# Performance work log

Hardware: AMD Instinct MI355X
Metric: run time of the kernel (lower is better)

Reference implementation:

```python
import jax, jax.numpy as jnp
import numpy as np

D_MODEL = 2048
N_HEADS = 32
N_KV_HEADS = 8
HEAD_DIM = D_MODEL // N_HEADS
N_REP = N_HEADS // N_KV_HEADS
ROPE_BASE = 10000.0


def _rope_tables(seq_len, dim, dtype):
    inv_freq = 1.0 / (ROPE_BASE ** (jnp.arange(0, dim, 2, dtype=jnp.float32) / dim))
    t = jnp.arange(seq_len, dtype=jnp.float32)
    freqs = jnp.einsum('i,j->ij', t, inv_freq)          # [S, dim/2]
    emb = jnp.concatenate([freqs, freqs], axis=-1)      # [S, dim]
    return jnp.cos(emb).astype(dtype), jnp.sin(emb).astype(dtype)


def _apply_rotation(x, cos, sin):
    # x: [B, H, S, D]; cos/sin: [S, D] broadcast over B,H
    half = x.shape[-1] // 2
    x1, x2 = x[..., :half], x[..., half:]
    rot = jnp.concatenate([-x2, x1], axis=-1)
    return rot * sin + x * cos


def setup_inputs() -> dict:
    key = jax.random.key(0)
    kx, kq, kk, kv, ko = jax.random.split(key, 5)
    B, S = 2, 2048
    scale_in = 1.0 / np.sqrt(D_MODEL)
    x = jax.random.normal(kx, (B, S, D_MODEL), dtype=jnp.float32)
    Wq = jax.random.normal(kq, (N_HEADS * HEAD_DIM, D_MODEL), dtype=jnp.float32) * scale_in
    Wk = jax.random.normal(kk, (N_KV_HEADS * HEAD_DIM, D_MODEL), dtype=jnp.float32) * scale_in
    Wv = jax.random.normal(kv, (N_KV_HEADS * HEAD_DIM, D_MODEL), dtype=jnp.float32) * scale_in
    Wo = jax.random.normal(ko, (D_MODEL, N_HEADS * HEAD_DIM), dtype=jnp.float32) * scale_in
    # additive causal mask, broadcast over batch and heads
    neg = jnp.float32(-1e9)
    causal = jnp.triu(jnp.full((S, S), neg, dtype=jnp.float32), k=1)[None, None]
    return {"x": x, "Wq": Wq, "Wk": Wk, "Wv": Wv, "Wo": Wo, "mask": causal}


def reference(x, Wq, Wk, Wv, Wo, mask):
    B, S, _ = x.shape
    q = (x @ Wq.T).reshape(B, S, N_HEADS, HEAD_DIM).transpose(0, 2, 1, 3)      # [B,H,S,D]
    k = (x @ Wk.T).reshape(B, S, N_KV_HEADS, HEAD_DIM).transpose(0, 2, 1, 3)   # [B,Hkv,S,D]
    v = (x @ Wv.T).reshape(B, S, N_KV_HEADS, HEAD_DIM).transpose(0, 2, 1, 3)
    cos, sin = _rope_tables(S, HEAD_DIM, x.dtype)
    q = _apply_rotation(q, cos, sin)
    k = _apply_rotation(k, cos, sin)
    # repeat_kv: [B,Hkv,S,D] -> [B,Hkv*n_rep,S,D]
    k = jnp.repeat(k, N_REP, axis=1)
    v = jnp.repeat(v, N_REP, axis=1)
    scale = jnp.sqrt(jnp.float32(HEAD_DIM)).astype(x.dtype)
    scores = jnp.einsum('bhqd,bhkd->bhqk', q, k) / scale
    scores = scores + mask
    attn = jax.nn.softmax(scores.astype(jnp.float32), axis=-1).astype(q.dtype)
    out = jnp.einsum('bhqk,bhkd->bhqd', attn, v)
    out = out.transpose(0, 2, 1, 3).reshape(B, S, N_HEADS * HEAD_DIM)
    return out @ Wo.T
```

## Files before the change

kernel.cpp:

```cpp
#include <hip/hip_runtime.h>


typedef __bf16 bf16x8 __attribute__((ext_vector_type(8)));
typedef __bf16 bf16x4 __attribute__((ext_vector_type(4)));
typedef float f32x4 __attribute__((ext_vector_type(4)));

__device__ inline f32x4 mfma16(bf16x8 a, bf16x8 b, f32x4 c) {
    return __builtin_amdgcn_mfma_f32_16x16x32_bf16(a, b, c, 0, 0, 0);
}

__device__ inline void gld16(const __bf16* g, __bf16* l) {
    __builtin_amdgcn_global_load_lds(
        (const __attribute__((address_space(1))) void*)g,
        (__attribute__((address_space(3))) void*)l, 16, 0, 0);
}

__device__ inline bf16x4 pk4(float a, float b, float c, float d) {
    bf16x4 r; r[0] = (__bf16)a; r[1] = (__bf16)b; r[2] = (__bf16)c; r[3] = (__bf16)d;
    return r;
}

#define SCALE_Q 0.18033688011112042f
#define L2IF    0.4152410118609203f
#define INV2PI  0.15915494309189535f

__global__ void cvt4_kernel(const float* __restrict__ x,  const float* __restrict__ wq,
                            const float* __restrict__ wk, const float* __restrict__ wv,
                            __bf16* __restrict__ xb, __bf16* __restrict__ wqkvb)
{
    int i = blockIdx.x * blockDim.x + threadIdx.x;
    const float* src; __bf16* dst;
    if (i < 2097152)      { src = x  + (size_t)i * 4;  dst = xb + (size_t)i * 4; }
    else if (i < 3145728) { int j = i - 2097152; src = wq + (size_t)j * 4; dst = wqkvb + (size_t)j * 4; }
    else if (i < 3407872) { int j = i - 3145728; src = wk + (size_t)j * 4; dst = wqkvb + 4194304 + (size_t)j * 4; }
    else                  { int j = i - 3407872; src = wv + (size_t)j * 4; dst = wqkvb + 5242880 + (size_t)j * 4; }
    float4 f = *(const float4*)src;
    *(bf16x4*)dst = pk4(f.x, f.y, f.z, f.w);
}

__global__ void cvt_kernel(const float* __restrict__ in, __bf16* __restrict__ out, int n4)
{
    int i = blockIdx.x * blockDim.x + threadIdx.x;
    if (i >= n4) return;
    float4 f = ((const float4*)in)[i];
    ((bf16x4*)out)[i] = pk4(f.x, f.y, f.z, f.w);
}

template<bool ROPE, bool OUT_F32>
__global__ __launch_bounds__(512, 2) void gemm256(
    const __bf16* __restrict__ A, const __bf16* __restrict__ Bw,
    void* __restrict__ Cv, int M, int N, int K)
{
    __shared__ __bf16 LA[2][16384];
    __shared__ __bf16 LB[2][16384];
    const int tid  = threadIdx.x;
    const int lane = tid & 63;
    const int w    = tid >> 6;
    const int lm   = lane & 15;
    const int quad = lane >> 4;
    const int wr   = w >> 2;
    const int wc   = w & 3;

    int bx, by;
    {
        int nwg = gridDim.x * gridDim.y;
        int id  = blockIdx.x + gridDim.x * blockIdx.y;
        int q   = nwg >> 3;
        int swz = (id & 7) * q + (id >> 3);
        by = swz / gridDim.x;
        bx = swz - by * gridDim.x;
    }
    const int m0 = by * 256;
    const int n0 = bx * 256;
    const int NT = K >> 6;

    const int srow = tid >> 3;
    const int scol = ((tid & 7) ^ (srow & 7)) * 8;
    const int ldst = tid * 8;
    const __bf16* ga = A  + (size_t)(m0 + srow) * K + scol;
    const __bf16* gb = Bw + (size_t)(n0 + srow) * K + scol;

    auto STA = [&](int bf, int r, int u) {
        gld16(ga + (size_t)r * K + u * 64, &LA[bf][r * 64 + ldst]);
    };
    auto STB = [&](int bf, int r, int u) {
        gld16(gb + (size_t)r * K + u * 64, &LB[bf][r * 64 + ldst]);
    };

    f32x4 acc[8][4];
    #pragma unroll
    for (int i = 0; i < 8; ++i)
        #pragma unroll
        for (int j = 0; j < 4; ++j)
            acc[i][j] = (f32x4){0.f, 0.f, 0.f, 0.f};

    const int axo = (wr * 128 + lm) * 64;
    const int bxo = (wc * 64  + lm) * 64;
    const int ks0 = ((quad * 8)      ^ ((lm & 7) * 8));
    const int ks1 = ((32 + quad * 8) ^ ((lm & 7) * 8));

    STA(0, 0, 0); STA(0, 64, 0); STA(0, 128, 0); STA(0, 192, 0);
    STB(0, 0, 0); STB(0, 64, 0); STB(0, 128, 0); STB(0, 192, 0);
    STA(1, 0, 1); STA(1, 128, 1); STB(1, 0, 1); STA(1, 64, 1); STB(1, 64, 1);
    asm volatile("s_waitcnt vmcnt(5)" ::: "memory");
    __builtin_amdgcn_s_barrier();
    asm volatile("" ::: "memory");

    bf16x8 Af[4][2], Bf[4][2];
    for (int t = 0; t < NT; ++t) {
        const int b = t & 1;
        const __bf16* la = LA[b];
        const __bf16* lb = LB[b];
        #pragma unroll
        for (int mi = 0; mi < 4; ++mi) {
            Af[mi][0] = *(const bf16x8*)(la + axo + mi * 1024 + ks0);
            Af[mi][1] = *(const bf16x8*)(la + axo + mi * 1024 + ks1);
        }
        #pragma unroll
        for (int ni = 0; ni < 2; ++ni) {
            Bf[ni][0] = *(const bf16x8*)(lb + bxo + ni * 1024 + ks0);
            Bf[ni][1] = *(const bf16x8*)(lb + bxo + ni * 1024 + ks1);
        }
        if (t + 1 < NT) { STA(b ^ 1, 192, t + 1); STB(b ^ 1, 128, t + 1); }
        __builtin_amdgcn_s_barrier();
        asm volatile("s_waitcnt lgkmcnt(0)" ::: "memory");
        __builtin_amdgcn_s_setprio(1);
        #pragma unroll
        for (int mi = 0; mi < 4; ++mi)
            #pragma unroll
            for (int ni = 0; ni < 2; ++ni) {
                acc[mi][ni] = mfma16(Af[mi][0], Bf[ni][0], acc[mi][ni]);
                acc[mi][ni] = mfma16(Af[mi][1], Bf[ni][1], acc[mi][ni]);
            }
        __builtin_amdgcn_s_setprio(0);
        __builtin_amdgcn_s_barrier();
        #pragma unroll
        for (int ni = 2; ni < 4; ++ni) {
            Bf[ni][0] = *(const bf16x8*)(lb + bxo + ni * 1024 + ks0);
            Bf[ni][1] = *(const bf16x8*)(lb + bxo + ni * 1024 + ks1);
        }
        if (t + 1 < NT) STB(b ^ 1, 192, t + 1);
        if (t + 2 < NT) STA(b, 0, t + 2);
        __builtin_amdgcn_s_barrier();
        asm volatile("s_waitcnt lgkmcnt(0)" ::: "memory");
        __builtin_amdgcn_s_setprio(1);
        #pragma unroll
        for (int mi = 0; mi < 4; ++mi)
            #pragma unroll
            for (int ni = 2; ni < 4; ++ni) {
                acc[mi][ni] = mfma16(Af[mi][0], Bf[ni][0], acc[mi][ni]);
                acc[mi][ni] = mfma16(Af[mi][1], Bf[ni][1], acc[mi][ni]);
            }
        __builtin_amdgcn_s_setprio(0);
        __builtin_amdgcn_s_barrier();
        #pragma unroll
        for (int mi = 0; mi < 4; ++mi) {
            Af[mi][0] = *(const bf16x8*)(la + axo + (mi + 4) * 1024 + ks0);
            Af[mi][1] = *(const bf16x8*)(la + axo + (mi + 4) * 1024 + ks1);
        }
        if (t + 2 < NT) { STA(b, 128, t + 2); STB(b, 0, t + 2); }
        __builtin_amdgcn_s_barrier();
        asm volatile("s_waitcnt lgkmcnt(0)" ::: "memory");
        __builtin_amdgcn_s_setprio(1);
        #pragma unroll
        for (int mi = 0; mi < 4; ++mi)
            #pragma unroll
            for (int ni = 0; ni < 2; ++ni) {
                acc[mi + 4][ni] = mfma16(Af[mi][0], Bf[ni][0], acc[mi + 4][ni]);
                acc[mi + 4][ni] = mfma16(Af[mi][1], Bf[ni][1], acc[mi + 4][ni]);
            }
        __builtin_amdgcn_s_setprio(0);
        __builtin_amdgcn_s_barrier();
        if (t + 2 < NT) { STA(b, 64, t + 2); STB(b, 64, t + 2); }
        __builtin_amdgcn_s_barrier();
        __builtin_amdgcn_s_setprio(1);
        #pragma unroll
        for (int mi = 0; mi < 4; ++mi)
            #pragma unroll
            for (int ni = 2; ni < 4; ++ni) {
                acc[mi + 4][ni] = mfma16(Af[mi][0], Bf[ni][0], acc[mi + 4][ni]);
                acc[mi + 4][ni] = mfma16(Af[mi][1], Bf[ni][1], acc[mi + 4][ni]);
            }
        __builtin_amdgcn_s_setprio(0);
        if (t < NT - 2)       asm volatile("s_waitcnt vmcnt(5)" ::: "memory");
        else if (t == NT - 2) asm volatile("s_waitcnt vmcnt(0)" ::: "memory");
        __builtin_amdgcn_s_barrier();
        asm volatile("" ::: "memory");
    }

    float sc = 1.0f;
    if (ROPE) {
        const int colbase = n0 + wc * 64;
        const int region  = (colbase < 2048) ? 0 : (colbase < 2560 ? 1 : 2);
        if (region < 2) {
            if (region == 0) sc = SCALE_Q;
            float invr[2];
            invr[0] = exp2f(-(float)lm        * L2IF) * INV2PI;
            invr[1] = exp2f(-(float)(16 + lm) * L2IF) * INV2PI;
            #pragma unroll
            for (int i = 0; i < 8; ++i)
                #pragma unroll
                for (int r = 0; r < 4; ++r) {
                    float tt = (float)((m0 + wr * 128 + i * 16 + quad * 4 + r) & 2047);
                    #pragma unroll
                    for (int jp = 0; jp < 2; ++jp) {
                        float aR = tt * invr[jp];
                        aR -= floorf(aR);
                        float cs = __builtin_amdgcn_cosf(aR);
                        float sn = __builtin_amdgcn_sinf(aR);
                        float x1 = acc[i][jp][r], x2 = acc[i][jp + 2][r];
                        acc[i][jp][r]     = x1 * cs - x2 * sn;
                        acc[i][jp + 2][r] = x2 * cs + x1 * sn;
                    }
                }
        }
    }

    #pragma unroll
    for (int i = 0; i < 8; ++i)
        #pragma unroll
        for (int j = 0; j < 4; ++j)
            #pragma unroll
            for (int r = 0; r < 4; ++r) {
                int row = m0 + wr * 128 + i * 16 + quad * 4 + r;
                int col = n0 + wc * 64 + j * 16 + lm;
                if (OUT_F32)
                    ((float*)Cv)[(size_t)row * N + col] = acc[i][j][r];
                else
                    ((__bf16*)Cv)[(size_t)row * N + col] = (__bf16)(acc[i][j][r] * sc);
            }
}

#define BK 32

template<bool ROPE, bool OUT_F32>
__global__ __launch_bounds__(256) void gemm_bt(
    const __bf16* __restrict__ A, const __bf16* __restrict__ Bw,
    void* __restrict__ Cv, int M, int N, int K)
{
    __shared__ __bf16 As[128 * BK];
    __shared__ __bf16 Bs[128 * BK];
    const int tid  = threadIdx.x;
    const int lane = tid & 63;
    const int w    = tid >> 6;
    const int lm   = lane & 15;
    const int quad = lane >> 4;
    const int wm   = (w >> 1) * 64;
    const int wn   = (w & 1) * 64;

    int bx, by;
    {
        int id  = blockIdx.x + gridDim.x * blockIdx.y;
        int xcd = id & 7;
        int j   = id >> 3;
        by = xcd * 4 + (j & 3);
        bx = j >> 2;
    }
    const int m0 = by * 128;
    const int n0 = bx * 128;

    f32x4 acc[4][4];
    #pragma unroll
    for (int i = 0; i < 4; ++i)
        #pragma unroll
        for (int j = 0; j < 4; ++j)
            acc[i][j] = (f32x4){0.f, 0.f, 0.f, 0.f};

    const int srow = tid >> 2;
    const int sc8  = (tid & 3) * 8;
    const __bf16* gA0 = A  + (size_t)(m0 + srow) * K + sc8;
    const __bf16* gA1 = gA0 + (size_t)64 * K;
    const __bf16* gB0 = Bw + (size_t)(n0 + srow) * K + sc8;
    const __bf16* gB1 = gB0 + (size_t)64 * K;
    __bf16* lA0 = &As[srow * BK + sc8];
    __bf16* lA1 = &As[(srow + 64) * BK + sc8];
    __bf16* lB0 = &Bs[srow * BK + sc8];
    __bf16* lB1 = &Bs[(srow + 64) * BK + sc8];

    for (int k0 = 0; k0 < K; k0 += BK) {
        gld16(gA0 + k0, lA0);
        gld16(gA1 + k0, lA1);
        gld16(gB0 + k0, lB0);
        gld16(gB1 + k0, lB1);
        __syncthreads();

        bf16x8 af[4], bfr[4];
        #pragma unroll
        for (int i = 0; i < 4; ++i)
            af[i] = *(const bf16x8*)&As[(wm + i * 16 + lm) * BK + quad * 8];
        #pragma unroll
        for (int j = 0; j < 4; ++j)
            bfr[j] = *(const bf16x8*)&Bs[(wn + j * 16 + lm) * BK + quad * 8];
        #pragma unroll
        for (int i = 0; i < 4; ++i)
            #pragma unroll
            for (int j = 0; j < 4; ++j)
                acc[i][j] = mfma16(af[i], bfr[j], acc[i][j]);
        __syncthreads();
    }

    float sc = 1.0f;
    if (ROPE) {
        const int colbase = n0 + wn;
        const int region  = (colbase < 2048) ? 0 : (colbase < 2560 ? 1 : 2);
        if (region < 2) {
            if (region == 0) sc = SCALE_Q;
            float invr[2];
            invr[0] = exp2f(-(float)lm        * L2IF) * INV2PI;
            invr[1] = exp2f(-(float)(16 + lm) * L2IF) * INV2PI;
            #pragma unroll
            for (int i = 0; i < 4; ++i)
                #pragma unroll
                for (int r = 0; r < 4; ++r) {
                    float t = (float)((m0 + wm + i * 16 + quad * 4 + r) & 2047);
                    #pragma unroll
                    for (int jp = 0; jp < 2; ++jp) {
                        float a = t * invr[jp];
                        a -= floorf(a);
                        float cs = __builtin_amdgcn_cosf(a);
                        float sn = __builtin_amdgcn_sinf(a);
                        float x1 = acc[i][jp][r], x2 = acc[i][jp + 2][r];
                        acc[i][jp][r]     = x1 * cs - x2 * sn;
                        acc[i][jp + 2][r] = x2 * cs + x1 * sn;
                    }
                }
        }
    }

    #pragma unroll
    for (int i = 0; i < 4; ++i)
        #pragma unroll
        for (int j = 0; j < 4; ++j)
            #pragma unroll
            for (int r = 0; r < 4; ++r) {
                int row = m0 + wm + i * 16 + quad * 4 + r;
                int col = n0 + wn + j * 16 + lm;
                if (OUT_F32)
                    ((float*)Cv)[(size_t)row * N + col] = acc[i][j][r];
                else
                    ((__bf16*)Cv)[(size_t)row * N + col] = (__bf16)(acc[i][j][r] * sc);
            }
}

__global__ __launch_bounds__(256) void transpose_kernel(
    const __bf16* __restrict__ in, __bf16* __restrict__ out, int rowstride)
{
    __shared__ __bf16 T[64][72];
    const int t0 = blockIdx.x * 64;
    const int d0 = blockIdx.y * 64;
    const int r = threadIdx.x >> 2, c = (threadIdx.x & 3) * 16;
    *(int4*)&T[r][c]     = *(const int4*)(in + (size_t)(t0 + r) * rowstride + d0 + c);
    *(int4*)&T[r][c + 8] = *(const int4*)(in + (size_t)(t0 + r) * rowstride + d0 + c + 8);
    __syncthreads();
    bf16x8 o0, o1;
    #pragma unroll
    for (int i = 0; i < 8; ++i) { o0[i] = T[c + i][r]; o1[i] = T[c + 8 + i][r]; }
    *(bf16x8*)(out + (size_t)(d0 + r) * 4096 + t0 + c)     = o0;
    *(bf16x8*)(out + (size_t)(d0 + r) * 4096 + t0 + c + 8) = o1;
}

#define RS  72
#define PKS 72

__device__ inline void attn_tile(
    const bf16x8 (&qf)[2], f32x4 (&oacc)[4], float& l,
    int qbase, int k0, int w, int lm, int quad,
    const __bf16* Ks, const __bf16* Vs, __bf16* Ptw)
{
    f32x4 st[4];
    #pragma unroll
    for (int n = 0; n < 4; ++n)
        st[n] = (f32x4){0.f, 0.f, 0.f, 0.f};

    #pragma unroll
    for (int n = 0; n < 4; ++n) {
        bf16x8 kf0 = *(const bf16x8*)&Ks[(n * 16 + lm) * RS + quad * 8];
        bf16x8 kf1 = *(const bf16x8*)&Ks[(n * 16 + lm) * RS + 32 + quad * 8];
        st[n] = mfma16(kf0, qf[0], st[n]);
        st[n] = mfma16(kf1, qf[1], st[n]);
    }

    const int qi = qbase + w * 16 + lm;
    const bool any_mask = (k0 + 63 > qbase + w * 16);
    #pragma unroll
    for (int n = 0; n < 4; ++n) {
        const int kv0 = k0 + n * 16 + quad * 4;
        float e0, e1, e2, e3;
        if (any_mask) {
            e0 = (kv0     > qi) ? 0.f : __builtin_amdgcn_exp2f(st[n][0]);
            e1 = (kv0 + 1 > qi) ? 0.f : __builtin_amdgcn_exp2f(st[n][1]);
            e2 = (kv0 + 2 > qi) ? 0.f : __builtin_amdgcn_exp2f(st[n][2]);
            e3 = (kv0 + 3 > qi) ? 0.f : __builtin_amdgcn_exp2f(st[n][3]);
        } else {
            e0 = __builtin_amdgcn_exp2f(st[n][0]); e1 = __builtin_amdgcn_exp2f(st[n][1]);
            e2 = __builtin_amdgcn_exp2f(st[n][2]); e3 = __builtin_amdgcn_exp2f(st[n][3]);
        }
        l += (e0 + e1) + (e2 + e3);
        *(bf16x4*)&Ptw[lm * PKS + n * 16 + quad * 4] = pk4(e0, e1, e2, e3);
    }

    bf16x8 pf0 = *(const bf16x8*)&Ptw[lm * PKS + quad * 8];
    bf16x8 pf1 = *(const bf16x8*)&Ptw[lm * PKS + 32 + quad * 8];
    #pragma unroll
    for (int dt = 0; dt < 4; ++dt) {
        bf16x8 vf0 = *(const bf16x8*)&Vs[(dt * 16 + lm) * RS + quad * 8];
        bf16x8 vf1 = *(const bf16x8*)&Vs[(dt * 16 + lm) * RS + 32 + quad * 8];
        oacc[dt] = mfma16(vf0, pf0, oacc[dt]);
        oacc[dt] = mfma16(vf1, pf1, oacc[dt]);
    }
}

__device__ inline void attn_tile2(
    const bf16x8 (&qfA)[2], const bf16x8 (&qfB)[2],
    f32x4 (&oA)[4], f32x4 (&oB)[4], float& lA, float& lB,
    int qbA, int k0, int w, int lm, int quad,
    const __bf16* Ks, const __bf16* Vs, __bf16* PtA, __bf16* PtB)
{
    f32x4 stA[4], stB[4];
    #pragma unroll
    for (int n = 0; n < 4; ++n) {
        stA[n] = (f32x4){0.f, 0.f, 0.f, 0.f};
        stB[n] = (f32x4){0.f, 0.f, 0.f, 0.f};
    }

    #pragma unroll
    for (int n = 0; n < 4; ++n) {
        bf16x8 kf0 = *(const bf16x8*)&Ks[(n * 16 + lm) * RS + quad * 8];
        bf16x8 kf1 = *(const bf16x8*)&Ks[(n * 16 + lm) * RS + 32 + quad * 8];
        stB[n] = mfma16(kf0, qfB[0], stB[n]);
        stB[n] = mfma16(kf1, qfB[1], stB[n]);
        stA[n] = mfma16(kf0, qfA[0], stA[n]);
        stA[n] = mfma16(kf1, qfA[1], stA[n]);
    }

    #pragma unroll
    for (int n = 0; n < 4; ++n) {
        float e0 = __builtin_amdgcn_exp2f(stB[n][0]);
        float e1 = __builtin_amdgcn_exp2f(stB[n][1]);
        float e2 = __builtin_amdgcn_exp2f(stB[n][2]);
        float e3 = __builtin_amdgcn_exp2f(stB[n][3]);
        lB += (e0 + e1) + (e2 + e3);
        *(bf16x4*)&PtB[lm * PKS + n * 16 + quad * 4] = pk4(e0, e1, e2, e3);
    }

    const int qiA = qbA + w * 16 + lm;
    const bool maskA = (k0 + 63 > qbA + w * 16);
    #pragma unroll
    for (int n = 0; n < 4; ++n) {
        const int kv0 = k0 + n * 16 + quad * 4;
        float e0, e1, e2, e3;
        if (maskA) {
            e0 = (kv0     > qiA) ? 0.f : __builtin_amdgcn_exp2f(stA[n][0]);
            e1 = (kv0 + 1 > qiA) ? 0.f : __builtin_amdgcn_exp2f(stA[n][1]);
            e2 = (kv0 + 2 > qiA) ? 0.f : __builtin_amdgcn_exp2f(stA[n][2]);
            e3 = (kv0 + 3 > qiA) ? 0.f : __builtin_amdgcn_exp2f(stA[n][3]);
        } else {
            e0 = __builtin_amdgcn_exp2f(stA[n][0]); e1 = __builtin_amdgcn_exp2f(stA[n][1]);
            e2 = __builtin_amdgcn_exp2f(stA[n][2]); e3 = __builtin_amdgcn_exp2f(stA[n][3]);
        }
        lA += (e0 + e1) + (e2 + e3);
        *(bf16x4*)&PtA[lm * PKS + n * 16 + quad * 4] = pk4(e0, e1, e2, e3);
    }

    bf16x8 pB0 = *(const bf16x8*)&PtB[lm * PKS + quad * 8];
    bf16x8 pB1 = *(const bf16x8*)&PtB[lm * PKS + 32 + quad * 8];
    bf16x8 pA0 = *(const bf16x8*)&PtA[lm * PKS + quad * 8];
    bf16x8 pA1 = *(const bf16x8*)&PtA[lm * PKS + 32 + quad * 8];
    #pragma unroll
    for (int dt = 0; dt < 4; ++dt) {
        bf16x8 vf0 = *(const bf16x8*)&Vs[(dt * 16 + lm) * RS + quad * 8];
        bf16x8 vf1 = *(const bf16x8*)&Vs[(dt * 16 + lm) * RS + 32 + quad * 8];
        oB[dt] = mfma16(vf0, pB0, oB[dt]);
        oB[dt] = mfma16(vf1, pB1, oB[dt]);
        oA[dt] = mfma16(vf0, pA0, oA[dt]);
        oA[dt] = mfma16(vf1, pA1, oA[dt]);
    }
}

__device__ inline void attn_epilogue(
    f32x4 (&oacc)[4], float l,
    int qbase, int w, int lm, int quad, int b, int h, __bf16* o)
{
    float ls = l;
    ls += __shfl_xor(ls, 16);
    ls += __shfl_xor(ls, 32);
    float rinv = 1.0f / ls;
    const size_t rowbase = (size_t)(b * 2048 + qbase + w * 16 + lm) * 2048 + h * 64;
    #pragma unroll
    for (int dt = 0; dt < 4; ++dt) {
        *(bf16x4*)(o + rowbase + dt * 16 + quad * 4) =
            pk4(oacc[dt][0] * rinv, oacc[dt][1] * rinv,
                oacc[dt][2] * rinv, oacc[dt][3] * rinv);
    }
}

__global__ __launch_bounds__(512, 4) void attn_kernel(
    const __bf16* __restrict__ qkv, const __bf16* __restrict__ vt,
    __bf16* __restrict__ o)
{
    __shared__ __bf16 Ks[2][64 * RS];
    __shared__ __bf16 Vs[2][64 * RS];
    __shared__ __bf16 Pt[8][2][16 * PKS];
    const int tid  = threadIdx.x;
    const int w    = tid >> 6;
    const int lane = tid & 63;
    const int lm   = lane & 15;
    const int quad = lane >> 4;
    const int p = blockIdx.x, h = blockIdx.y, b = blockIdx.z;
    const int kvh = h >> 2;
    const int qbA = p * 128, qbB = (15 - p) * 128;
    const int ntA = 2 * p + 2, ntB = 32 - 2 * p;
    __bf16* PtwB = &Pt[w][0][0];
    __bf16* PtwA = &Pt[w][1][0];

    bf16x8 qfA[2], qfB[2];
    #pragma unroll
    for (int kh = 0; kh < 2; ++kh) {
        qfA[kh] = *(const bf16x8*)(qkv + (size_t)(b * 2048 + qbA + w * 16 + lm) * 3072
                                      + h * 64 + kh * 32 + quad * 8);
        qfB[kh] = *(const bf16x8*)(qkv + (size_t)(b * 2048 + qbB + w * 16 + lm) * 3072
                                      + h * 64 + kh * 32 + quad * 8);
    }

    f32x4 oA[4], oB[4];
    float lA = 0.f, lB = 0.f;
    #pragma unroll
    for (int j = 0; j < 4; ++j) {
        oA[j] = (f32x4){0.f, 0.f, 0.f, 0.f};
        oB[j] = (f32x4){0.f, 0.f, 0.f, 0.f};
    }

    const int srow = tid >> 3;
    const int scol = (tid & 7) * 8;
    const __bf16* kbase = qkv + (size_t)(b * 2048) * 3072 + 2048 + kvh * 64;
    const __bf16* vbase = vt  + (size_t)(kvh * 64 + srow) * 4096 + b * 2048;

    int4 kr0, vr0;
    kr0 = *(const int4*)(kbase + (size_t)srow * 3072 + scol);
    vr0 = *(const int4*)(vbase + scol);

    for (int kt = 0; kt < ntB; ++kt) {
        const int c = kt & 1;
        const int k0 = kt * 64;
        *(int4*)&Ks[c][srow * RS + scol] = kr0;
        *(int4*)&Vs[c][srow * RS + scol] = vr0;
        if (kt + 1 < ntB) {
            kr0 = *(const int4*)(kbase + (size_t)(k0 + 64 + srow) * 3072 + scol);
            vr0 = *(const int4*)(vbase + k0 + 64 + scol);
        }
        __syncthreads();
        if (kt < ntA)
            attn_tile2(qfA, qfB, oA, oB, lA, lB, qbA, k0, w, lm, quad,
                       Ks[c], Vs[c], PtwA, PtwB);
        else
            attn_tile(qfB, oB, lB, qbB, k0, w, lm, quad, Ks[c], Vs[c], PtwB);
    }

    attn_epilogue(oA, lA, qbA, w, lm, quad, b, h, o);
    attn_epilogue(oB, lB, qbB, w, lm, quad, b, h, o);
}

extern "C" void kernel_launch(void* const* d_in, const int* in_sizes, int n_in,
                              void* d_out, int out_size, void* d_ws, size_t ws_size,
                              hipStream_t stream)
{
    const float* x  = (const float*)d_in[0];
    const float* Wq = (const float*)d_in[1];
    const float* Wk = (const float*)d_in[2];
    const float* Wv = (const float*)d_in[3];
    const float* Wo = (const float*)d_in[4];

    const size_t Mi = 1u << 20;
    char* ob = (char*)d_out;
    __bf16* xb    = (__bf16*)ob;
    __bf16* wqkvb = (__bf16*)(ob + 16 * Mi);
    __bf16* vt    = (__bf16*)(ob + 28 * Mi);
    char* ws = (char*)d_ws;
    __bf16* qkvc = (__bf16*)ws;
    __bf16* aws  = (__bf16*)(ws + 24 * Mi);
    __bf16* wob  = (__bf16*)ws;

    dim3 blk(256);
    cvt4_kernel<<<14336, blk, 0, stream>>>(x, Wq, Wk, Wv, xb, wqkvb);
    gemm256<true, false><<<dim3(12, 16), dim3(512), 0, stream>>>(xb, wqkvb, qkvc, 4096, 3072, 2048);
    transpose_kernel<<<dim3(64, 8), blk, 0, stream>>>(qkvc + 2560, vt, 3072);
    attn_kernel<<<dim3(8, 32, 2), dim3(512), 0, stream>>>(qkvc, vt, aws);
    cvt_kernel<<<4096, blk, 0, stream>>>(Wo, wob, 1048576);
    gemm_bt<false, true><<<dim3(16, 32), blk, 0, stream>>>(aws, wob, d_out, 4096, 2048, 2048);
}
```

Baseline: 310.7 us.

## Rewrite output GEMM as double-buffered 256x128 kernel and XOR-swizzle attention LDS

```diff
diff --git a/kernel.cpp b/kernel.cpp
--- a/kernel.cpp
+++ b/kernel.cpp
@@ -231,33 +231,43 @@
             }
 }
 
-#define BK 32
-
-template<bool ROPE, bool OUT_F32>
-__global__ __launch_bounds__(256) void gemm_bt(
+__global__ __launch_bounds__(512, 2) void gemm_o(
     const __bf16* __restrict__ A, const __bf16* __restrict__ Bw,
-    void* __restrict__ Cv, int M, int N, int K)
-{
-    __shared__ __bf16 As[128 * BK];
-    __shared__ __bf16 Bs[128 * BK];
+    float* __restrict__ C, int M, int N, int K)
+{
+    __shared__ __bf16 LA[2][16384];
+    __shared__ __bf16 LB[2][8192];
     const int tid  = threadIdx.x;
     const int lane = tid & 63;
     const int w    = tid >> 6;
     const int lm   = lane & 15;
     const int quad = lane >> 4;
-    const int wm   = (w >> 1) * 64;
-    const int wn   = (w & 1) * 64;
+    const int wr   = w >> 1;
+    const int wc   = w & 1;
 
     int bx, by;
     {
         int id  = blockIdx.x + gridDim.x * blockIdx.y;
-        int xcd = id & 7;
-        int j   = id >> 3;
-        by = xcd * 4 + (j & 3);
-        bx = j >> 2;
-    }
-    const int m0 = by * 128;
+        int swz = (id & 7) * 32 + (id >> 3);
+        by = swz >> 4;
+        bx = swz & 15;
+    }
+    const int m0 = by * 256;
     const int n0 = bx * 128;
+    const int NT = K >> 6;
+
+    const int srow = tid >> 3;
+    const int scol = ((tid & 7) ^ (srow & 7)) * 8;
+    const int ldst = tid * 8;
+    const __bf16* ga = A  + (size_t)(m0 + srow) * K + scol;
+    const __bf16* gb = Bw + (size_t)(n0 + srow) * K + scol;
+
+    auto STA = [&](int bf, int r, int u) {
+        gld16(ga + (size_t)r * K + u * 64, &LA[bf][r * 64 + ldst]);
+    };
+    auto STB = [&](int bf, int r, int u) {
+        gld16(gb + (size_t)r * K + u * 64, &LB[bf][r * 64 + ldst]);
+    };
 
     f32x4 acc[4][4];
     #pragma unroll
@@ -266,79 +276,109 @@
         for (int j = 0; j < 4; ++j)
             acc[i][j] = (f32x4){0.f, 0.f, 0.f, 0.f};
 
-    const int srow = tid >> 2;
-    const int sc8  = (tid & 3) * 8;
-    const __bf16* gA0 = A  + (size_t)(m0 + srow) * K + sc8;
-    const __bf16* gA1 = gA0 + (size_t)64 * K;
-    const __bf16* gB0 = Bw + (size_t)(n0 + srow) * K + sc8;
-    const __bf16* gB1 = gB0 + (size_t)64 * K;
-    __bf16* lA0 = &As[srow * BK + sc8];
-    __bf16* lA1 = &As[(srow + 64) * BK + sc8];
-    __bf16* lB0 = &Bs[srow * BK + sc8];
-    __bf16* lB1 = &Bs[(srow + 64) * BK + sc8];
-
-    for (int k0 = 0; k0 < K; k0 += BK) {
-        gld16(gA0 + k0, lA0);
-        gld16(gA1 + k0, lA1);
-        gld16(gB0 + k0, lB0);
-        gld16(gB1 + k0, lB1);
-        __syncthreads();
-
-        bf16x8 af[4], bfr[4];
-        #pragma unroll
-        for (int i = 0; i < 4; ++i)
-            af[i] = *(const bf16x8*)&As[(wm + i * 16 + lm) * BK + quad * 8];
+    const int axo = (wr * 64 + lm) * 64;
+    const int bxo = (wc * 64 + lm) * 64;
+    const int ks0 = ((quad * 8)      ^ ((lm & 7) * 8));
+    const int ks1 = ((32 + quad * 8) ^ ((lm & 7) * 8));
+
+    STA(0, 0, 0); STA(0, 64, 0); STA(0, 128, 0); STA(0, 192, 0);
+    STB(0, 0, 0); STB(0, 64, 0);
+    STA(1, 0, 1); STA(1, 64, 1); STA(1, 128, 1); STA(1, 192, 1);
+    STB(1, 0, 1); STB(1, 64, 1);
+    asm volatile("s_waitcnt vmcnt(6)" ::: "memory");
+    __builtin_amdgcn_s_barrier();
+    asm volatile("" ::: "memory");
+
+    bf16x8 Af[4][2], Bf[4][2];
+    for (int t = 0; t < NT; ++t) {
+        const int b = t & 1;
+        const __bf16* la = LA[b];
+        const __bf16* lb = LB[b];
+        #pragma unroll
+        for (int mi = 0; mi < 2; ++mi) {
+            Af[mi][0] = *(const bf16x8*)(la + axo + mi * 1024 + ks0);
+            Af[mi][1] = *(const bf16x8*)(la + axo + mi * 1024 + ks1);
+        }
+        #pragma unroll
+        for (int ni = 0; ni < 2; ++ni) {
+            Bf[ni][0] = *(const bf16x8*)(lb + bxo + ni * 1024 + ks0);
+            Bf[ni][1] = *(const bf16x8*)(lb + bxo + ni * 1024 + ks1);
+        }
+        __builtin_amdgcn_s_barrier();
+        asm volatile("s_waitcnt lgkmcnt(0)" ::: "memory");
+        __builtin_amdgcn_s_setprio(1);
+        #pragma unroll
+        for (int mi = 0; mi < 2; ++mi)
+            #pragma unroll
+            for (int ni = 0; ni < 2; ++ni) {
+                acc[mi][ni] = mfma16(Af[mi][0], Bf[ni][0], acc[mi][ni]);
+                acc[mi][ni] = mfma16(Af[mi][1], Bf[ni][1], acc[mi][ni]);
+            }
+        __builtin_amdgcn_s_setprio(0);
+        __builtin_amdgcn_s_barrier();
+        #pragma unroll
+        for (int ni = 2; ni < 4; ++ni) {
+            Bf[ni][0] = *(const bf16x8*)(lb + bxo + ni * 1024 + ks0);
+            Bf[ni][1] = *(const bf16x8*)(lb + bxo + ni * 1024 + ks1);
+        }
+        __builtin_amdgcn_s_barrier();
+        asm volatile("s_waitcnt lgkmcnt(0)" ::: "memory");
+        __builtin_amdgcn_s_setprio(1);
+        #pragma unroll
+        for (int mi = 0; mi < 2; ++mi)
+            #pragma unroll
+            for (int ni = 2; ni < 4; ++ni) {
+                acc[mi][ni] = mfma16(Af[mi][0], Bf[ni][0], acc[mi][ni]);
+                acc[mi][ni] = mfma16(Af[mi][1], Bf[ni][1], acc[mi][ni]);
+            }
+        __builtin_amdgcn_s_setprio(0);
+        __builtin_amdgcn_s_barrier();
+        #pragma unroll
+        for (int mi = 2; mi < 4; ++mi) {
+            Af[mi][0] = *(const bf16x8*)(la + axo + mi * 1024 + ks0);
+            Af[mi][1] = *(const bf16x8*)(la + axo + mi * 1024 + ks1);
+        }
+        if (t + 2 < NT) { STB(b, 0, t + 2); STB(b, 64, t + 2); }
+        __builtin_amdgcn_s_barrier();
+        asm volatile("s_waitcnt lgkmcnt(0)" ::: "memory");
+        __builtin_amdgcn_s_setprio(1);
+        #pragma unroll
+        for (int mi = 2; mi < 4; ++mi)
+            #pragma unroll
+            for (int ni = 0; ni < 2; ++ni) {
+                acc[mi][ni] = mfma16(Af[mi][0], Bf[ni][0], acc[mi][ni]);
+                acc[mi][ni] = mfma16(Af[mi][1], Bf[ni][1], acc[mi][ni]);
+            }
+        __builtin_amdgcn_s_setprio(0);
+        __builtin_amdgcn_s_barrier();
+        if (t + 2 < NT) {
+            STA(b, 0, t + 2); STA(b, 64, t + 2);
+            STA(b, 128, t + 2); STA(b, 192, t + 2);
+        }
+        __builtin_amdgcn_s_setprio(1);
+        #pragma unroll
+        for (int mi = 2; mi < 4; ++mi)
+            #pragma unroll
+            for (int ni = 2; ni < 4; ++ni) {
+                acc[mi][ni] = mfma16(Af[mi][0], Bf[ni][0], acc[mi][ni]);
+                acc[mi][ni] = mfma16(Af[mi][1], Bf[ni][1], acc[mi][ni]);
+            }
+        __builtin_amdgcn_s_setprio(0);
+        if (t < NT - 2) asm volatile("s_waitcnt vmcnt(6)" ::: "memory");
+        else            asm volatile("s_waitcnt vmcnt(0)" ::: "memory");
+        __builtin_amdgcn_s_barrier();
+        asm volatile("" ::: "memory");
+    }
+
+    #pragma unroll
+    for (int i = 0; i < 4; ++i)
         #pragma unroll
         for (int j = 0; j < 4; ++j)
-            bfr[j] = *(const bf16x8*)&Bs[(wn + j * 16 + lm) * BK + quad * 8];
-        #pragma unroll
-        for (int i = 0; i < 4; ++i)
-            #pragma unroll
-            for (int j = 0; j < 4; ++j)
-                acc[i][j] = mfma16(af[i], bfr[j], acc[i][j]);
-        __syncthreads();
-    }
-
-    float sc = 1.0f;
-    if (ROPE) {
-        const int colbase = n0 + wn;
-        const int region  = (colbase < 2048) ? 0 : (colbase < 2560 ? 1 : 2);
-        if (region < 2) {
-            if (region == 0) sc = SCALE_Q;
-            float invr[2];
-            invr[0] = exp2f(-(float)lm        * L2IF) * INV2PI;
-            invr[1] = exp2f(-(float)(16 + lm) * L2IF) * INV2PI;
-            #pragma unroll
-            for (int i = 0; i < 4; ++i)
-                #pragma unroll
-                for (int r = 0; r < 4; ++r) {
-                    float t = (float)((m0 + wm + i * 16 + quad * 4 + r) & 2047);
-                    #pragma unroll
-                    for (int jp = 0; jp < 2; ++jp) {
-                        float a = t * invr[jp];
-                        a -= floorf(a);
-                        float cs = __builtin_amdgcn_cosf(a);
-                        float sn = __builtin_amdgcn_sinf(a);
-                        float x1 = acc[i][jp][r], x2 = acc[i][jp + 2][r];
-                        acc[i][jp][r]     = x1 * cs - x2 * sn;
-                        acc[i][jp + 2][r] = x2 * cs + x1 * sn;
-                    }
-                }
-        }
-    }
-
-    #pragma unroll
-    for (int i = 0; i < 4; ++i)
-        #pragma unroll
-        for (int j = 0; j < 4; ++j)
             #pragma unroll
             for (int r = 0; r < 4; ++r) {
-                int row = m0 + wm + i * 16 + quad * 4 + r;
-                int col = n0 + wn + j * 16 + lm;
-                if (OUT_F32)
-                    ((float*)Cv)[(size_t)row * N + col] = acc[i][j][r];
-                else
-                    ((__bf16*)Cv)[(size_t)row * N + col] = (__bf16)(acc[i][j][r] * sc);
+                int row = m0 + wr * 64 + i * 16 + quad * 4 + r;
+                int col = n0 + wc * 64 + j * 16 + lm;
+                C[(size_t)row * N + col] = acc[i][j][r];
             }
 }
 
@@ -359,14 +399,16 @@
     *(bf16x8*)(out + (size_t)(d0 + r) * 4096 + t0 + c + 8) = o1;
 }
 
-#define RS  72
-#define PKS 72
+#define RS  64
+#define PKS 64
 
 __device__ inline void attn_tile(
     const bf16x8 (&qf)[2], f32x4 (&oacc)[4], float& l,
     int qbase, int k0, int w, int lm, int quad,
     const __bf16* Ks, const __bf16* Vs, __bf16* Ptw)
 {
+    const int kb0 = (quad ^ (lm & 7)) * 8;
+    const int kb1 = ((quad + 4) ^ (lm & 7)) * 8;
     f32x4 st[4];
     #pragma unroll
     for (int n = 0; n < 4; ++n)
@@ -374,8 +416,8 @@
 
     #pragma unroll
     for (int n = 0; n < 4; ++n) {
-        bf16x8 kf0 = *(const bf16x8*)&Ks[(n * 16 + lm) * RS + quad * 8];
-        bf16x8 kf1 = *(const bf16x8*)&Ks[(n * 16 + lm) * RS + 32 + quad * 8];
+        bf16x8 kf0 = *(const bf16x8*)&Ks[(n * 16 + lm) * RS + kb0];
+        bf16x8 kf1 = *(const bf16x8*)&Ks[(n * 16 + lm) * RS + kb1];
         st[n] = mfma16(kf0, qf[0], st[n]);
         st[n] = mfma16(kf1, qf[1], st[n]);
     }
@@ -396,15 +438,16 @@
             e2 = __builtin_amdgcn_exp2f(st[n][2]); e3 = __builtin_amdgcn_exp2f(st[n][3]);
         }
         l += (e0 + e1) + (e2 + e3);
-        *(bf16x4*)&Ptw[lm * PKS + n * 16 + quad * 4] = pk4(e0, e1, e2, e3);
-    }
-
-    bf16x8 pf0 = *(const bf16x8*)&Ptw[lm * PKS + quad * 8];
-    bf16x8 pf1 = *(const bf16x8*)&Ptw[lm * PKS + 32 + quad * 8];
+        *(bf16x4*)&Ptw[lm * PKS + ((n * 4 + quad) ^ ((lm & 7) << 1)) * 4] =
+            pk4(e0, e1, e2, e3);
+    }
+
+    bf16x8 pf0 = *(const bf16x8*)&Ptw[lm * PKS + kb0];
+    bf16x8 pf1 = *(const bf16x8*)&Ptw[lm * PKS + kb1];
     #pragma unroll
     for (int dt = 0; dt < 4; ++dt) {
-        bf16x8 vf0 = *(const bf16x8*)&Vs[(dt * 16 + lm) * RS + quad * 8];
-        bf16x8 vf1 = *(const bf16x8*)&Vs[(dt * 16 + lm) * RS + 32 + quad * 8];
+        bf16x8 vf0 = *(const bf16x8*)&Vs[(dt * 16 + lm) * RS + kb0];
+        bf16x8 vf1 = *(const bf16x8*)&Vs[(dt * 16 + lm) * RS + kb1];
         oacc[dt] = mfma16(vf0, pf0, oacc[dt]);
         oacc[dt] = mfma16(vf1, pf1, oacc[dt]);
     }
@@ -416,6 +459,8 @@
     int qbA, int k0, int w, int lm, int quad,
     const __bf16* Ks, const __bf16* Vs, __bf16* PtA, __bf16* PtB)
 {
+    const int kb0 = (quad ^ (lm & 7)) * 8;
+    const int kb1 = ((quad + 4) ^ (lm & 7)) * 8;
     f32x4 stA[4], stB[4];
     #pragma unroll
     for (int n = 0; n < 4; ++n) {
@@ -425,8 +470,8 @@
 
     #pragma unroll
     for (int n = 0; n < 4; ++n) {
-        bf16x8 kf0 = *(const bf16x8*)&Ks[(n * 16 + lm) * RS + quad * 8];
-        bf16x8 kf1 = *(const bf16x8*)&Ks[(n * 16 + lm) * RS + 32 + quad * 8];
+        bf16x8 kf0 = *(const bf16x8*)&Ks[(n * 16 + lm) * RS + kb0];
+        bf16x8 kf1 = *(const bf16x8*)&Ks[(n * 16 + lm) * RS + kb1];
         stB[n] = mfma16(kf0, qfB[0], stB[n]);
         stB[n] = mfma16(kf1, qfB[1], stB[n]);
         stA[n] = mfma16(kf0, qfA[0], stA[n]);
@@ -440,7 +485,8 @@
         float e2 = __builtin_amdgcn_exp2f(stB[n][2]);
         float e3 = __builtin_amdgcn_exp2f(stB[n][3]);
         lB += (e0 + e1) + (e2 + e3);
-        *(bf16x4*)&PtB[lm * PKS + n * 16 + quad * 4] = pk4(e0, e1, e2, e3);
+        *(bf16x4*)&PtB[lm * PKS + ((n * 4 + quad) ^ ((lm & 7) << 1)) * 4] =
+            pk4(e0, e1, e2, e3);
     }
 
     const int qiA = qbA + w * 16 + lm;
@@ -459,17 +505,18 @@
             e2 = __builtin_amdgcn_exp2f(stA[n][2]); e3 = __builtin_amdgcn_exp2f(stA[n][3]);
         }
         lA += (e0 + e1) + (e2 + e3);
-        *(bf16x4*)&PtA[lm * PKS + n * 16 + quad * 4] = pk4(e0, e1, e2, e3);
-    }
-
-    bf16x8 pB0 = *(const bf16x8*)&PtB[lm * PKS + quad * 8];
-    bf16x8 pB1 = *(const bf16x8*)&PtB[lm * PKS + 32 + quad * 8];
-    bf16x8 pA0 = *(const bf16x8*)&PtA[lm * PKS + quad * 8];
-    bf16x8 pA1 = *(const bf16x8*)&PtA[lm * PKS + 32 + quad * 8];
+        *(bf16x4*)&PtA[lm * PKS + ((n * 4 + quad) ^ ((lm & 7) << 1)) * 4] =
+            pk4(e0, e1, e2, e3);
+    }
+
+    bf16x8 pB0 = *(const bf16x8*)&PtB[lm * PKS + kb0];
+    bf16x8 pB1 = *(const bf16x8*)&PtB[lm * PKS + kb1];
+    bf16x8 pA0 = *(const bf16x8*)&PtA[lm * PKS + kb0];
+    bf16x8 pA1 = *(const bf16x8*)&PtA[lm * PKS + kb1];
     #pragma unroll
     for (int dt = 0; dt < 4; ++dt) {
-        bf16x8 vf0 = *(const bf16x8*)&Vs[(dt * 16 + lm) * RS + quad * 8];
-        bf16x8 vf1 = *(const bf16x8*)&Vs[(dt * 16 + lm) * RS + 32 + quad * 8];
+        bf16x8 vf0 = *(const bf16x8*)&Vs[(dt * 16 + lm) * RS + kb0];
+        bf16x8 vf1 = *(const bf16x8*)&Vs[(dt * 16 + lm) * RS + kb1];
         oB[dt] = mfma16(vf0, pB0, oB[dt]);
         oB[dt] = mfma16(vf1, pB1, oB[dt]);
         oA[dt] = mfma16(vf0, pA0, oA[dt]);
@@ -531,22 +578,23 @@
     }
 
     const int srow = tid >> 3;
-    const int scol = (tid & 7) * 8;
+    const int scg  = (tid & 7) * 8;
+    const int scl  = (((tid & 7) ^ (srow & 7))) * 8;
     const __bf16* kbase = qkv + (size_t)(b * 2048) * 3072 + 2048 + kvh * 64;
     const __bf16* vbase = vt  + (size_t)(kvh * 64 + srow) * 4096 + b * 2048;
 
     int4 kr0, vr0;
-    kr0 = *(const int4*)(kbase + (size_t)srow * 3072 + scol);
-    vr0 = *(const int4*)(vbase + scol);
+    kr0 = *(const int4*)(kbase + (size_t)srow * 3072 + scg);
+    vr0 = *(const int4*)(vbase + scg);
 
     for (int kt = 0; kt < ntB; ++kt) {
         const int c = kt & 1;
         const int k0 = kt * 64;
-        *(int4*)&Ks[c][srow * RS + scol] = kr0;
-        *(int4*)&Vs[c][srow * RS + scol] = vr0;
+        *(int4*)&Ks[c][srow * RS + scl] = kr0;
+        *(int4*)&Vs[c][srow * RS + scl] = vr0;
         if (kt + 1 < ntB) {
-            kr0 = *(const int4*)(kbase + (size_t)(k0 + 64 + srow) * 3072 + scol);
-            vr0 = *(const int4*)(vbase + k0 + 64 + scol);
+            kr0 = *(const int4*)(kbase + (size_t)(k0 + 64 + srow) * 3072 + scg);
+            vr0 = *(const int4*)(vbase + k0 + 64 + scg);
         }
         __syncthreads();
         if (kt < ntA)
@@ -586,5 +634,5 @@
     transpose_kernel<<<dim3(64, 8), blk, 0, stream>>>(qkvc + 2560, vt, 3072);
     attn_kernel<<<dim3(8, 32, 2), dim3(512), 0, stream>>>(qkvc, vt, aws);
     cvt_kernel<<<4096, blk, 0, stream>>>(Wo, wob, 1048576);
-    gemm_bt<false, true><<<dim3(16, 32), blk, 0, stream>>>(aws, wob, d_out, 4096, 2048, 2048);
-}
+    gemm_o<<<dim3(16, 16), dim3(512), 0, stream>>>(aws, wob, (float*)d_out, 4096, 2048, 2048);
+}
```

Result: faster. 292.7 us (-5.8%).
